# Optimization experiments

Measured on AMD Instinct MI355X. Metric: run time of the kernel, lower is better.

## Reference

```python
import jax, jax.numpy as jnp
import numpy as np
import math

D_MODEL = 1024
FEAT = 16            # feature_dim
HEADS = 16
HEAD_DIM = D_MODEL // HEADS          # 64
EXP = 1 + FEAT + FEAT * FEAT         # 273, expanded (Taylor) feature dim
BATCH = 4
SEQ = 2048


def taylor_exp(x):
    """2nd-order Taylor feature map: [1, x/d^{1/4}, (x ox x)/(sqrt(2)*sqrt(d))]."""
    d = x.shape[-1]
    r2 = math.sqrt(2.0)
    rd = math.sqrt(d)
    rrd = math.sqrt(rd)
    x2 = (x[..., :, None] * x[..., None, :]).reshape(*x.shape[:-1], d * d) / r2
    return jnp.concatenate([jnp.ones_like(x[..., :1]), x / rrd, x2 / rd], axis=-1)


def setup_inputs() -> dict:
    key = jax.random.key(0)
    ks = jax.random.split(key, 9)
    s_in = 1.0 / math.sqrt(D_MODEL)
    inp = {
        "x": jax.random.normal(ks[0], (BATCH, SEQ, D_MODEL), dtype=jnp.float32),
        "kv_state": jnp.zeros((BATCH, HEADS, EXP, HEAD_DIM), dtype=jnp.float32),
        "k_state": jnp.zeros((BATCH, HEADS, EXP), dtype=jnp.float32),
        # Linear params stored as [in, out] (y = x @ W + b)
        "Wq": jax.random.normal(ks[1], (D_MODEL, FEAT * HEADS), dtype=jnp.float32) * s_in,
        "bq": jnp.zeros((FEAT * HEADS,), dtype=jnp.float32),
        "Wk": jax.random.normal(ks[2], (D_MODEL, FEAT * HEADS), dtype=jnp.float32) * s_in,
        "bk": jnp.zeros((FEAT * HEADS,), dtype=jnp.float32),
        "Wv": jax.random.normal(ks[3], (D_MODEL, HEAD_DIM * HEADS), dtype=jnp.float32) * s_in,
        "bv": jnp.zeros((HEAD_DIM * HEADS,), dtype=jnp.float32),
        "Wo": jax.random.normal(ks[4], (HEADS * HEAD_DIM, D_MODEL), dtype=jnp.float32) * s_in,
        "bo": jnp.zeros((D_MODEL,), dtype=jnp.float32),
    }
    return inp


def _forward(x, kv_state, k_state, Wq, bq, Wk, bk, Wv, bv, Wo, bo):
    b, l, _ = x.shape
    # projections -> b h l d
    q = (x @ Wq + bq).reshape(b, l, HEADS, FEAT).transpose(0, 2, 1, 3)
    k = (x @ Wk + bk).reshape(b, l, HEADS, FEAT).transpose(0, 2, 1, 3)
    v = (x @ Wv + bv).reshape(b, l, HEADS, HEAD_DIM).transpose(0, 2, 1, 3)
    q = taylor_exp(q)  # b h l EXP
    k = taylor_exp(k)  # b h l EXP

    # scan over time: carry (kv_state [b,h,EXP,hd], k_state [b,h,EXP])
    qs = jnp.moveaxis(q, 2, 0)  # l b h EXP
    ks = jnp.moveaxis(k, 2, 0)  # l b h EXP
    vs = jnp.moveaxis(v, 2, 0)  # l b h hd

    def step(carry, qkv_t):
        kv, kst = carry
        q_t, k_t, v_t = qkv_t
        kv = kv + k_t[..., :, None] * v_t[..., None, :]   # b h EXP hd
        kst = kst + k_t                                    # b h EXP
        num = jnp.einsum('bhd,bhdc->bhc', q_t, kv)
        den = jnp.einsum('bhd,bhd->bh', q_t, kst) + 1e-6
        return (kv, kst), num / den[..., None]

    (kv_f, kst_f), outs = jax.lax.scan(step, (kv_state, k_state), (qs, ks, vs))
    # outs: l b h hd -> b l (h hd)
    y = jnp.moveaxis(outs, 0, 1).reshape(b, l, HEADS * HEAD_DIM)
    y = y @ Wo + bo  # dropout is identity in eval mode
    return y, kv_f, kst_f


def reference(x, kv_state, k_state, Wq, bq, Wk, bk, Wv, bv, Wo, bo):
    return _forward(x, kv_state, k_state, Wq, bq, Wk, bk, Wv, bv, Wo, bo)
```

## Files before the change

### kernel.cpp

```cpp
#include <hip/hip_runtime.h>

typedef unsigned short u16;
typedef __attribute__((ext_vector_type(8))) short bf16x8;
typedef __attribute__((ext_vector_type(4))) float f32x4;

#define BATCH 4
#define SEQ   2048
#define DM    1024
#define HEADS 16
#define FEAT  16
#define HD    64
#define EXPD  273
#define EXPP  288
#define CHK   128
#define NC    16
#define BH    64
#define QKS   512
#define MROWS 8192
#define C2    0.17677669529663687f

__device__ __forceinline__ u16 f2b(float f) {
  union { float f; unsigned u; } v; v.f = f;
  unsigned u = v.u;
  return (u16)((u + 0x7fffu + ((u >> 16) & 1u)) >> 16);
}
__device__ __forceinline__ float b2f(u16 s) {
  union { unsigned u; float f; } v; v.u = ((unsigned)s) << 16; return v.f;
}
__device__ __forceinline__ unsigned pk2b(float a, float b) {
  unsigned r;
  asm("v_cvt_pk_bf16_f32 %0, %1, %2" : "=v"(r) : "v"(a), "v"(b));
  return r;
}

typedef const unsigned int __attribute__((address_space(1)))* gas1;
typedef unsigned int __attribute__((address_space(3)))* las3;
__device__ __forceinline__ void gl_lds16(const u16* g, u16* l) {
  __builtin_amdgcn_global_load_lds((gas1)(const void*)g, (las3)(void*)l, 16, 0, 0);
}

__global__ __launch_bounds__(256) void prep(const float* __restrict__ x, u16* __restrict__ xb,
                                            const float* __restrict__ Wq, const float* __restrict__ Wk,
                                            const float* __restrict__ Wv, const float* __restrict__ Wo,
                                            u16* __restrict__ wqkvT, u16* __restrict__ woT,
                                            const float* __restrict__ bq, const float* __restrict__ bk,
                                            const float* __restrict__ bv, float* __restrict__ bias_all) {
  __shared__ float tile[32][33];
  int id = blockIdx.x;
  if (id < 8192) {
    int i = id * 256 + threadIdx.x;
    float4 v = ((const float4*)x)[i];
    uint2 r; r.x = pk2b(v.x, v.y); r.y = pk2b(v.z, v.w);
    ((uint2*)xb)[i] = r;
    return;
  }
  id -= 8192;
  if (id < 2560) {
    const float* src; u16* dst; int N, t;
    if (id < 256)       { src = Wq; dst = wqkvT;            N = 256;  t = id; }
    else if (id < 512)  { src = Wk; dst = wqkvT + 256 * DM; N = 256;  t = id - 256; }
    else if (id < 1536) { src = Wv; dst = wqkvT + 512 * DM; N = 1024; t = id - 512; }
    else                { src = Wo; dst = woT;              N = 1024; t = id - 1536; }
    int nt = N / 32;
    int n0 = (t % nt) * 32, k0 = (t / nt) * 32;
    int tx = threadIdx.x & 31, ty = threadIdx.x >> 5;
    for (int i = ty; i < 32; i += 8)
      tile[i][tx] = src[(size_t)(k0 + i) * N + n0 + tx];
    __syncthreads();
    for (int i = ty; i < 32; i += 8)
      dst[(size_t)(n0 + i) * DM + k0 + tx] = f2b(tile[tx][i]);
    return;
  }
  id -= 2560;
  int i = id * 256 + threadIdx.x;
  float v;
  if (i < 256) v = bq[i];
  else if (i < 512) v = bk[i - 256];
  else v = bv[i - 512];
  bias_all[i] = v;
}

__global__ __launch_bounds__(256, 2) void gemmQKV(const u16* __restrict__ A, const u16* __restrict__ BT,
                                                  const float* __restrict__ bias,
                                                  float* __restrict__ qkw, u16* __restrict__ vbT) {
  __shared__ __align__(16) u16 As[2][128 * 32];
  __shared__ __align__(16) u16 Bs[2][192 * 32];
  const int tid = threadIdx.x;
  const int wave = tid >> 6, lane = tid & 63, qd = lane >> 4, ln = lane & 15;
  const int wr = (wave >> 1) * 64, wc = (wave & 1) * 96;
  const int m0 = blockIdx.y * 128, n0 = blockIdx.x * 192;
  const int K = DM;
  f32x4 acc[4][6];
#pragma unroll
  for (int i = 0; i < 4; i++)
#pragma unroll
    for (int j = 0; j < 6; j++) acc[i][j] = (f32x4){0.f, 0.f, 0.f, 0.f};
  const int sr = tid >> 2;
  const int scs = (((tid & 3) ^ ((sr >> 1) & 3))) * 8;
  const u16* gA0 = A + (size_t)(m0 + sr) * K + scs;
  const u16* gA1 = gA0 + (size_t)64 * K;
  const u16* gB0 = BT + (size_t)(n0 + sr) * K + scs;
  auto stage = [&](int buf, int kk) {
    gl_lds16(gA0 + kk, &As[buf][wave * 512]);
    gl_lds16(gA1 + kk, &As[buf][2048 + wave * 512]);
    gl_lds16(gB0 + kk,                   &Bs[buf][wave * 512]);
    gl_lds16(gB0 + (size_t)64 * K + kk,  &Bs[buf][2048 + wave * 512]);
    gl_lds16(gB0 + (size_t)128 * K + kk, &Bs[buf][4096 + wave * 512]);
  };
  const int swz = ((ln >> 1) & 3) << 3;
  auto compute = [&](int buf) {
    bf16x8 af[4], bf[6];
#pragma unroll
    for (int t = 0; t < 4; t++)
      af[t] = *(const bf16x8*)&As[buf][(wr + t * 16 + ln) * 32 + ((qd * 8) ^ swz)];
#pragma unroll
    for (int u = 0; u < 6; u++)
      bf[u] = *(const bf16x8*)&Bs[buf][(wc + u * 16 + ln) * 32 + ((qd * 8) ^ swz)];
#pragma unroll
    for (int mt = 0; mt < 4; mt++)
#pragma unroll
      for (int nt = 0; nt < 6; nt++)
        acc[mt][nt] = __builtin_amdgcn_mfma_f32_16x16x32_bf16(af[mt], bf[nt], acc[mt][nt], 0, 0, 0);
  };
  stage(0, 0);
  int buf = 0;
  for (int kk = 32; kk < K; kk += 32) {
    stage(buf ^ 1, kk);
    asm volatile("s_waitcnt vmcnt(5)" ::: "memory");
    __builtin_amdgcn_s_barrier();
    asm volatile("" ::: "memory");
    compute(buf);
    asm volatile("" ::: "memory");
    __builtin_amdgcn_s_barrier();
    buf ^= 1;
  }
  asm volatile("s_waitcnt vmcnt(0)" ::: "memory");
  __builtin_amdgcn_s_barrier();
  asm volatile("" ::: "memory");
  compute(buf);
#pragma unroll
  for (int nt = 0; nt < 6; nt++) {
    int col = n0 + wc + nt * 16 + ln;
    float bv = bias[col];
    if (col < 512) {
#pragma unroll
      for (int mt = 0; mt < 4; mt++)
#pragma unroll
        for (int r = 0; r < 4; r++) {
          int row = m0 + wr + mt * 16 + qd * 4 + r;
          qkw[(size_t)row * QKS + col] = acc[mt][nt][r] + bv;
        }
    } else {
      int vcol = col - 512;
#pragma unroll
      for (int mt = 0; mt < 4; mt++) {
        uint2 pp;
        pp.x = pk2b(acc[mt][nt][0] + bv, acc[mt][nt][1] + bv);
        pp.y = pk2b(acc[mt][nt][2] + bv, acc[mt][nt][3] + bv);
        int row0 = m0 + wr + mt * 16 + qd * 4;
        *(uint2*)&vbT[(size_t)vcol * MROWS + row0] = pp;
      }
    }
  }
}

__global__ __launch_bounds__(256, 3) void gemm128(const u16* __restrict__ A, const u16* __restrict__ BT,
                                                  const float* __restrict__ bias, int M, int N, int K,
                                                  float* __restrict__ outF) {
  __shared__ __align__(16) u16 As[2][128 * 32];
  __shared__ __align__(16) u16 Bs[2][128 * 32];
  const int tid = threadIdx.x;
  const int wave = tid >> 6, lane = tid & 63, qd = lane >> 4, ln = lane & 15;
  const int wr = (wave >> 1) * 64, wc = (wave & 1) * 64;
  const int m0 = blockIdx.y * 128, n0 = blockIdx.x * 128;
  f32x4 acc[4][4];
#pragma unroll
  for (int i = 0; i < 4; i++)
#pragma unroll
    for (int j = 0; j < 4; j++) acc[i][j] = (f32x4){0.f, 0.f, 0.f, 0.f};
  const int sr = tid >> 2;
  const int scs = (((tid & 3) ^ ((sr >> 1) & 3))) * 8;
  const u16* gA0 = A + (size_t)(m0 + sr) * K + scs;
  const u16* gA1 = gA0 + (size_t)64 * K;
  const u16* gB0 = BT + (size_t)(n0 + sr) * K + scs;
  const u16* gB1 = gB0 + (size_t)64 * K;
  auto stage = [&](int buf, int kk) {
    gl_lds16(gA0 + kk, &As[buf][wave * 512]);
    gl_lds16(gA1 + kk, &As[buf][2048 + wave * 512]);
    gl_lds16(gB0 + kk, &Bs[buf][wave * 512]);
    gl_lds16(gB1 + kk, &Bs[buf][2048 + wave * 512]);
  };
  const int swz = ((ln >> 1) & 3) << 3;
  auto compute = [&](int buf) {
    bf16x8 af[4], bf[4];
#pragma unroll
    for (int t = 0; t < 4; t++)
      af[t] = *(const bf16x8*)&As[buf][(wr + t * 16 + ln) * 32 + ((qd * 8) ^ swz)];
#pragma unroll
    for (int u = 0; u < 4; u++)
      bf[u] = *(const bf16x8*)&Bs[buf][(wc + u * 16 + ln) * 32 + ((qd * 8) ^ swz)];
#pragma unroll
    for (int mt = 0; mt < 4; mt++)
#pragma unroll
      for (int nt = 0; nt < 4; nt++)
        acc[mt][nt] = __builtin_amdgcn_mfma_f32_16x16x32_bf16(af[mt], bf[nt], acc[mt][nt], 0, 0, 0);
  };
  stage(0, 0);
  int buf = 0;
  for (int kk = 32; kk < K; kk += 32) {
    stage(buf ^ 1, kk);
    asm volatile("s_waitcnt vmcnt(4)" ::: "memory");
    __builtin_amdgcn_s_barrier();
    asm volatile("" ::: "memory");
    compute(buf);
    asm volatile("" ::: "memory");
    __builtin_amdgcn_s_barrier();
    buf ^= 1;
  }
  asm volatile("s_waitcnt vmcnt(0)" ::: "memory");
  __builtin_amdgcn_s_barrier();
  asm volatile("" ::: "memory");
  compute(buf);
#pragma unroll
  for (int nt = 0; nt < 4; nt++) {
    int col = n0 + wc + nt * 16 + ln;
    float bv = bias[col];
#pragma unroll
    for (int mt = 0; mt < 4; mt++)
#pragma unroll
      for (int r = 0; r < 4; r++) {
        int row = m0 + wr + mt * 16 + qd * 4 + r;
        outF[(size_t)row * N + col] = acc[mt][nt][r] + bv;
      }
  }
}

template<int KT>
__device__ __forceinline__ void feat_row(const float* q16, int p, u16* dst) {
  float v[16];
  if (KT == 0 && p == 0) {
    v[0] = 1.0f;
#pragma unroll
    for (int j = 1; j < 16; j++) v[j] = 0.5f * q16[j - 1];
  } else if (KT == 0) {
    v[0] = 0.5f * q16[15];
    float wm = C2 * q16[0];
#pragma unroll
    for (int j = 1; j < 16; j++) v[j] = wm * q16[j - 1];
  } else {
    constexpr int c = 2 * KT;
    float wm = C2 * (p ? q16[c]     : q16[c - 1]);
    float w0 = C2 * (p ? q16[c - 1] : q16[c - 2]);
    v[0] = w0 * q16[15];
#pragma unroll
    for (int j = 1; j < 16; j++) v[j] = wm * q16[j - 1];
    if (KT == 8 && p) {
#pragma unroll
      for (int j = 1; j < 16; j++) v[j] = 0.f;
    }
  }
  unsigned w[8];
#pragma unroll
  for (int j = 0; j < 8; j++) w[j] = pk2b(v[2 * j], v[2 * j + 1]);
  *(uint4*)dst = *(uint4*)w;
  *(uint4*)(dst + 8) = *(uint4*)(w + 4);
}

template<int MTB>
__device__ __forceinline__ void kfeat(const float* k16, int p, int t2, u16 (*kfT)[16][136]) {
  float v[16];
  if (MTB == 0) {
    if (p == 0) {
      v[0] = 1.0f;
#pragma unroll
      for (int j = 1; j < 16; j++) v[j] = 0.5f * k16[j - 1];
    } else {
      float w0 = C2 * k16[0], wm = C2 * k16[1];
      v[0] = w0 * k16[15];
#pragma unroll
      for (int j = 1; j < 16; j++) v[j] = wm * k16[j - 1];
    }
  } else if (MTB == 1) {
    if (p == 0) {
      v[0] = 0.5f * k16[15];
      float wm = C2 * k16[0];
#pragma unroll
      for (int j = 1; j < 16; j++) v[j] = wm * k16[j - 1];
    } else {
      float w0 = C2 * k16[1], wm = C2 * k16[2];
      v[0] = w0 * k16[15];
#pragma unroll
      for (int j = 1; j < 16; j++) v[j] = wm * k16[j - 1];
    }
  } else {
    float wm = C2 * (p ? k16[MTB + 1] : k16[MTB - 1]);
    float w0 = C2 * (p ? k16[MTB]     : k16[MTB - 2]);
    v[0] = w0 * k16[15];
#pragma unroll
    for (int j = 1; j < 16; j++) v[j] = wm * k16[j - 1];
  }
  union { unsigned w[8]; u16 s[16]; } u;
#pragma unroll
  for (int j = 0; j < 8; j++) u.w[j] = pk2b(v[2 * j], v[2 * j + 1]);
  int b = 2 * p + (MTB & 1);
#pragma unroll
  for (int el = 0; el < 16; el++) kfT[b][el][t2] = u.s[el];
}

__global__ __launch_bounds__(256) void chunk_sums(const float* __restrict__ qkw, const u16* __restrict__ vbT,
                                                  u16* __restrict__ ckvT, float* __restrict__ ck) {
  __shared__ float kl[CHK][20];
  __shared__ __align__(16) u16 kfT[4][16][136];
  const int tid = threadIdx.x;
  const int bh = blockIdx.x / NC, c = blockIdx.x % NC;
  const int b = bh >> 4, h = bh & 15;
  const int wave = tid >> 6, lane = tid & 63, qd = lane >> 4, ln = lane & 15;
  const int t2 = tid >> 1, p = tid & 1;
  const size_t rowbase = (size_t)(b * SEQ + c * CHK);
  float k16[16];
  {
    const float* kp = &qkw[(rowbase + t2) * QKS + 256 + h * FEAT];
    float4 v0 = *(const float4*)kp, v1 = *(const float4*)(kp + 4);
    float4 v2 = *(const float4*)(kp + 8), v3 = *(const float4*)(kp + 12);
    k16[0] = v0.x; k16[1] = v0.y; k16[2] = v0.z; k16[3] = v0.w;
    k16[4] = v1.x; k16[5] = v1.y; k16[6] = v1.z; k16[7] = v1.w;
    k16[8] = v2.x; k16[9] = v2.y; k16[10] = v2.z; k16[11] = v2.w;
    k16[12] = v3.x; k16[13] = v3.y; k16[14] = v3.z; k16[15] = v3.w;
    float4 h0, h1;
    if (p == 0) { h0 = v0; h1 = v1; } else { h0 = v2; h1 = v3; }
    *(float4*)&kl[t2][p * 8] = h0;
    *(float4*)&kl[t2][p * 8 + 4] = h1;
  }
  uint4 bVv[4][4];
#pragma unroll
  for (int kk2 = 0; kk2 < 4; kk2++)
#pragma unroll
    for (int nt = 0; nt < 4; nt++)
      bVv[kk2][nt] = *(const uint4*)&vbT[(size_t)(h * HD + nt * 16 + ln) * MROWS +
                                         rowbase + kk2 * 32 + qd * 8];
  const size_t obase = (size_t)(bh * NC + c) * HD;
  auto mstore = [&](int mt, int bufw) {
    f32x4 acc[4];
#pragma unroll
    for (int nt = 0; nt < 4; nt++) acc[nt] = (f32x4){0.f, 0.f, 0.f, 0.f};
#pragma unroll
    for (int kk2 = 0; kk2 < 4; kk2++) {
      bf16x8 a = *(const bf16x8*)&kfT[bufw][ln][kk2 * 32 + qd * 8];
#pragma unroll
      for (int nt = 0; nt < 4; nt++) {
        bf16x8 bb = *(const bf16x8*)&bVv[kk2][nt];
        acc[nt] = __builtin_amdgcn_mfma_f32_16x16x32_bf16(a, bb, acc[nt], 0, 0, 0);
      }
    }
#pragma unroll
    for (int nt = 0; nt < 4; nt++) {
      uint2 pp;
      pp.x = pk2b(acc[nt][0], acc[nt][1]);
      pp.y = pk2b(acc[nt][2], acc[nt][3]);
      *(uint2*)&ckvT[(obase + nt * 16 + ln) * EXPP + mt * 16 + qd * 4] = pp;
    }
  };
  __syncthreads();
  kfeat<0>(k16, p, t2, kfT); kfeat<1>(k16, p, t2, kfT);
  __syncthreads();
  mstore(wave, wave);
  __syncthreads();
  kfeat<4>(k16, p, t2, kfT); kfeat<5>(k16, p, t2, kfT);
  __syncthreads();
  mstore(4 + wave, wave);
  __syncthreads();
  kfeat<8>(k16, p, t2, kfT); kfeat<9>(k16, p, t2, kfT);
  __syncthreads();
  mstore(8 + wave, wave);
  __syncthreads();
  kfeat<12>(k16, p, t2, kfT); kfeat<13>(k16, p, t2, kfT);
  __syncthreads();
  mstore(12 + wave, wave);
  __syncthreads();
  {
    float v[16];
    if (p == 0) {
      float w0 = C2 * k16[14], wm = C2 * k16[15];
      v[0] = w0 * k16[15];
#pragma unroll
      for (int j = 1; j < 16; j++) v[j] = wm * k16[j - 1];
    } else {
      v[0] = C2 * k16[15] * k16[15];
#pragma unroll
      for (int j = 1; j < 16; j++) v[j] = 0.f;
    }
    union { unsigned w[8]; u16 s[16]; } u;
#pragma unroll
    for (int j = 0; j < 8; j++) u.w[j] = pk2b(v[2 * j], v[2 * j + 1]);
#pragma unroll
    for (int el = 0; el < 16; el++) kfT[p][el][t2] = u.s[el];
  }
  __syncthreads();
  if (wave < 2) mstore(16 + wave, wave);
  for (int e = tid; e < EXPP; e += 256) {
    float s = 0.f;
    if (e == 0) s = (float)CHK;
    else if (e < 17) { float t = 0.f; for (int tt = 0; tt < CHK; tt++) t += kl[tt][e - 1]; s = 0.5f * t; }
    else if (e < EXPD) {
      int u = e - 17, i0 = u >> 4, j0 = u & 15; float t = 0.f;
      for (int tt = 0; tt < CHK; tt++) t += kl[tt][i0] * kl[tt][j0];
      s = C2 * t;
    }
    ck[(size_t)(bh * NC + c) * EXPP + e] = s;
  }
}

__global__ __launch_bounds__(256) void kv_prefix(u16* __restrict__ ckvT, const float* __restrict__ kv0,
                                                 float* __restrict__ out_kv,
                                                 float* __restrict__ ck, const float* __restrict__ k0,
                                                 float* __restrict__ out_k) {
  const int tid = threadIdx.x;
  const int bh = blockIdx.x / 10, eg = blockIdx.x % 10;
  if (eg == 9) {
    for (int e = tid; e < EXPP; e += 256) {
      float S = (e < EXPD) ? k0[(size_t)bh * EXPD + e] : 0.f;
      for (int c = 0; c < NC; c++) {
        size_t idx = ((size_t)bh * NC + c) * EXPP + e;
        float v = ck[idx];
        ck[idx] = S;
        S += v;
      }
      if (e < EXPD) out_k[(size_t)bh * EXPD + e] = S;
    }
    return;
  }
  const int hd = tid >> 2;
  const int e0 = eg * 32 + (tid & 3) * 8;
  float S[8];
#pragma unroll
  for (int j = 0; j < 8; j++) {
    int e = e0 + j;
    S[j] = (e < EXPD) ? kv0[((size_t)bh * EXPD + e) * HD + hd] : 0.f;
  }
  u16* base = ckvT + ((size_t)bh * NC * HD + hd) * EXPP + e0;
  const size_t cstride = (size_t)HD * EXPP;
  uint4 v0 = *(const uint4*)base;
  uint4 v1 = *(const uint4*)(base + cstride);
  for (int c = 0; c < NC; c++) {
    uint4 vn = v1;
    if (c + 2 < NC) vn = *(const uint4*)(base + (size_t)(c + 2) * cstride);
    union { uint4 q; unsigned w[4]; } pk;
#pragma unroll
    for (int j = 0; j < 4; j++) pk.w[j] = pk2b(S[2 * j], S[2 * j + 1]);
    *(uint4*)(base + (size_t)c * cstride) = pk.q;
    union { uint4 q; u16 s[8]; } vv; vv.q = v0;
#pragma unroll
    for (int j = 0; j < 8; j++) S[j] += b2f(vv.s[j]);
    v0 = v1; v1 = vn;
  }
#pragma unroll
  for (int j = 0; j < 8; j++) {
    int e = e0 + j;
    if (e < EXPD) out_kv[((size_t)bh * EXPD + e) * HD + hd] = S[j];
  }
}

__global__ __launch_bounds__(256) void out_chunk(const float* __restrict__ qkw, const u16* __restrict__ vbT,
                                                 const u16* __restrict__ ckvT, const float* __restrict__ ck,
                                                 u16* __restrict__ ob) {
  __shared__ __align__(16) u16 pool[19456];
  __shared__ float kstl[EXPP];
  __shared__ float denl[CHK];
  u16 (*qlb)[40]  = (u16(*)[40])pool;
  u16 (*klb)[32]  = (u16(*)[32])(pool + 5120);
  u16 (*qfs0)[40] = (u16(*)[40])(pool + 9216);
  u16 (*qfs1)[40] = (u16(*)[40])(pool + 14336);
  u16 (*alB)[72]  = (u16(*)[72])pool;
  u16 (*alA)[72]  = (u16(*)[72])(pool + 9216);
  const int tid = threadIdx.x;
  const int bh = blockIdx.x / NC, c = blockIdx.x % NC;
  const int b = bh >> 4, h = bh & 15;
  const int wave = tid >> 6, lane = tid & 63, qd = lane >> 4, ln = lane & 15;
  const int t2 = tid >> 1, p = tid & 1;
  const size_t rowbase = (size_t)(b * SEQ + c * CHK);
  float q16[16];
  {
    const float* qp = &qkw[(rowbase + t2) * QKS + h * FEAT];
    float4 v0 = *(const float4*)qp, v1 = *(const float4*)(qp + 4);
    float4 v2 = *(const float4*)(qp + 8), v3 = *(const float4*)(qp + 12);
    q16[0] = v0.x; q16[1] = v0.y; q16[2] = v0.z; q16[3] = v0.w;
    q16[4] = v1.x; q16[5] = v1.y; q16[6] = v1.z; q16[7] = v1.w;
    q16[8] = v2.x; q16[9] = v2.y; q16[10] = v2.z; q16[11] = v2.w;
    q16[12] = v3.x; q16[13] = v3.y; q16[14] = v3.z; q16[15] = v3.w;
    unsigned qw[4];
#pragma unroll
    for (int j = 0; j < 4; j++) qw[j] = pk2b(q16[p * 8 + 2 * j], q16[p * 8 + 2 * j + 1]);
    *(uint4*)&qlb[t2][p * 8] = *(uint4*)qw;
    *(uint4*)&qlb[t2][16 + p * 8] = (uint4){0u, 0u, 0u, 0u};
    const float* kp = &qkw[(rowbase + t2) * QKS + 256 + h * FEAT + p * 8];
    float4 k0v = *(const float4*)kp, k1v = *(const float4*)(kp + 4);
    unsigned kw[4] = {pk2b(k0v.x, k0v.y), pk2b(k0v.z, k0v.w),
                      pk2b(k1v.x, k1v.y), pk2b(k1v.z, k1v.w)};
    *(uint4*)&klb[t2][p * 8] = *(uint4*)kw;
    *(uint4*)&klb[t2][16 + p * 8] = (uint4){0u, 0u, 0u, 0u};
  }
  const size_t cbase = (size_t)(bh * NC + c);
  for (int e = tid; e < EXPP; e += 256) kstl[e] = ck[cbase * EXPP + e];
  const u16* sptr = ckvT + (cbase * HD + wave * 16 + ln) * EXPP + qd * 8;
  uint4 bSv[2];
  bSv[0] = *(const uint4*)(sptr + 0 * 32);
  feat_row<0>(q16, p, &qfs0[t2][p * 16]);
  f32x4 accO[8];
#pragma unroll
  for (int nt = 0; nt < 8; nt++) accO[nt] = (f32x4){0.f, 0.f, 0.f, 0.f};
#define KSTEP(KT, CUR, NXT)                                                                \
  {                                                                                        \
    __syncthreads();                                                                       \
    if ((KT) + 1 <= 8) bSv[((KT) + 1) & 1] = *(const uint4*)(sptr + ((KT) + 1) * 32);      \
    bf16x8 bQ0[4];                                                                         \
    _Pragma("unroll")                                                                      \
    for (int nt = 0; nt < 4; nt++) bQ0[nt] = *(const bf16x8*)&CUR[nt * 16 + ln][qd * 8];   \
    feat_row<(KT) + 1>(q16, p, &NXT[t2][p * 16]);                                          \
    bf16x8 aS = *(const bf16x8*)&bSv[(KT) & 1];                                            \
    _Pragma("unroll")                                                                      \
    for (int nt = 0; nt < 4; nt++)                                                         \
      accO[nt] = __builtin_amdgcn_mfma_f32_16x16x32_bf16(aS, bQ0[nt], accO[nt], 0, 0, 0);  \
    _Pragma("unroll")                                                                      \
    for (int nt = 4; nt < 8; nt++) {                                                       \
      bf16x8 bQ1 = *(const bf16x8*)&CUR[nt * 16 + ln][qd * 8];                             \
      accO[nt] = __builtin_amdgcn_mfma_f32_16x16x32_bf16(aS, bQ1, accO[nt], 0, 0, 0);      \
    }                                                                                      \
  }
  KSTEP(0, qfs0, qfs1) KSTEP(1, qfs1, qfs0) KSTEP(2, qfs0, qfs1) KSTEP(3, qfs1, qfs0)
  KSTEP(4, qfs0, qfs1) KSTEP(5, qfs1, qfs0) KSTEP(6, qfs0, qfs1) KSTEP(7, qfs1, qfs0)
#undef KSTEP
  {
    __syncthreads();
    bf16x8 aS = *(const bf16x8*)&bSv[0];
#pragma unroll
    for (int nt = 0; nt < 8; nt++) {
      bf16x8 bQ = *(const bf16x8*)&qfs0[nt * 16 + ln][qd * 8];
      accO[nt] = __builtin_amdgcn_mfma_f32_16x16x32_bf16(aS, bQ, accO[nt], 0, 0, 0);
    }
  }
  __syncthreads();
  float s_poly;
  {
    float s = 0.f;
#pragma unroll
    for (int i2 = 0; i2 < 8; i2++) {
      int i = p * 8 + i2;
      float inner = 0.f;
#pragma unroll
      for (int j = 0; j < 16; j++) inner += q16[j] * kstl[17 + i * 16 + j];
      s += q16[i] * inner;
    }
    s *= C2;
    float s1 = 0.f;
#pragma unroll
    for (int j2 = 0; j2 < 8; j2++) s1 += q16[p * 8 + j2] * kstl[1 + p * 8 + j2];
    s += 0.5f * s1;
    if (p == 0) s += kstl[0] + 1e-6f;
    s_poly = s;
  }
  {
    bf16x8 aK = *(const bf16x8*)&klb[wave * 16 + ln][qd * 8];
#pragma unroll
    for (int nn = 0; nn < 2; nn++) {
      f32x4 accU[4];
#pragma unroll
      for (int j = 0; j < 4; j++) {
        bf16x8 bQ = *(const bf16x8*)&qlb[(nn * 4 + j) * 16 + ln][qd * 8];
        accU[j] = __builtin_amdgcn_mfma_f32_16x16x32_bf16(aK, bQ, (f32x4){0.f, 0.f, 0.f, 0.f}, 0, 0, 0);
      }
#pragma unroll
      for (int j = 0; j < 4; j++) {
        int t = (nn * 4 + j) * 16 + ln, sb = wave * 16 + qd * 4;
        float scm[4];
#pragma unroll
        for (int r = 0; r < 4; r++) {
          float u = accU[j][r];
          float sc = 1.f + 0.25f * u + 0.03125f * u * u;
          scm[r] = (sb + r <= t) ? sc : 0.f;
        }
        uint2 pp; pp.x = pk2b(scm[0], scm[1]); pp.y = pk2b(scm[2], scm[3]);
        *(uint2*)&alA[t][sb] = pp;
      }
    }
  }
  {
    f32x4 accU[8];
    bf16x8 aK = *(const bf16x8*)&klb[(wave + 4) * 16 + ln][qd * 8];
#pragma unroll
    for (int nt = 0; nt < 8; nt++) {
      bf16x8 bQ = *(const bf16x8*)&qlb[nt * 16 + ln][qd * 8];
      accU[nt] = __builtin_amdgcn_mfma_f32_16x16x32_bf16(aK, bQ, (f32x4){0.f, 0.f, 0.f, 0.f}, 0, 0, 0);
    }
    uint4 bVv[4];
#pragma unroll
    for (int kk2 = 0; kk2 < 4; kk2++)
      bVv[kk2] = *(const uint4*)&vbT[(size_t)(h * HD + wave * 16 + ln) * MROWS +
                                     rowbase + kk2 * 32 + qd * 8];
    __syncthreads();
#pragma unroll
    for (int nt = 0; nt < 8; nt++) {
      int t = nt * 16 + ln, sbl = wave * 16 + qd * 4;
      float scm[4];
#pragma unroll
      for (int r = 0; r < 4; r++) {
        float u = accU[nt][r];
        float sc = 1.f + 0.25f * u + 0.03125f * u * u;
        scm[r] = (64 + sbl + r <= t) ? sc : 0.f;
      }
      uint2 pp; pp.x = pk2b(scm[0], scm[1]); pp.y = pk2b(scm[2], scm[3]);
      *(uint2*)&alB[t][sbl] = pp;
    }
    __syncthreads();
#pragma unroll
    for (int kk2 = 0; kk2 < 4; kk2++) {
      bf16x8 aV = *(const bf16x8*)&bVv[kk2];
#pragma unroll
      for (int nt = 0; nt < 8; nt++) {
        bf16x8 bA = (kk2 < 2) ? *(const bf16x8*)&alA[nt * 16 + ln][kk2 * 32 + qd * 8]
                              : *(const bf16x8*)&alB[nt * 16 + ln][(kk2 - 2) * 32 + qd * 8];
        accO[nt] = __builtin_amdgcn_mfma_f32_16x16x32_bf16(aV, bA, accO[nt], 0, 0, 0);
      }
    }
  }
  {
    const u16* arow = p ? &alB[t2][0] : &alA[t2][0];
    float da = 0.f;
#pragma unroll
    for (int sb = 0; sb < 8; sb++) {
      union { uint4 q; u16 hh[8]; } uu;
      uu.q = *(const uint4*)(arow + sb * 8);
#pragma unroll
      for (int j = 0; j < 8; j++) da += b2f(uu.hh[j]);
    }
    float s = s_poly + da;
    s += __shfl_xor(s, 1);
    if (p == 0) denl[t2] = s;
  }
  __syncthreads();
#pragma unroll
  for (int nt = 0; nt < 8; nt++) {
    int t = nt * 16 + ln;
    float rd = 1.0f / denl[t];
    uint2 pp;
    pp.x = pk2b(accO[nt][0] * rd, accO[nt][1] * rd);
    pp.y = pk2b(accO[nt][2] * rd, accO[nt][3] * rd);
    *(uint2*)&ob[(rowbase + t) * DM + h * HD + wave * 16 + qd * 4] = pp;
  }
}

extern "C" void kernel_launch(void* const* d_in, const int* in_sizes, int n_in,
                              void* d_out, int out_size, void* d_ws, size_t ws_size,
                              hipStream_t stream) {
  (void)in_sizes; (void)n_in; (void)out_size;
  const float* x   = (const float*)d_in[0];
  const float* kv0 = (const float*)d_in[1];
  const float* k0  = (const float*)d_in[2];
  const float* bq  = (const float*)d_in[4];
  const float* bk  = (const float*)d_in[6];
  const float* bv  = (const float*)d_in[8];
  const float* bo  = (const float*)d_in[10];
  float* out = (float*)d_out;
  char* ws = (char*)d_ws;
  size_t off = 0;
  auto take = [&](size_t bytes) { char* p = ws + off; off += (bytes + 255) & ~(size_t)255; return p; };
  u16*   xb     = (u16*)  take((size_t)BATCH * SEQ * DM * 2);
  u16*   wqkvT  = (u16*)  take((size_t)1536 * DM * 2);
  u16*   woT    = (u16*)  take((size_t)DM * DM * 2);
  float* bias_a = (float*)take((size_t)1536 * 4);
  float* qkw    = (float*)take((size_t)BATCH * SEQ * QKS * 4);
  u16*   vbT    = (u16*)  take((size_t)BATCH * SEQ * DM * 2);
  u16*   ckvT   = (u16*)  take((size_t)BH * NC * EXPP * HD * 2);
  float* ck     = (float*)take((size_t)BH * NC * EXPP * 4);
  u16*   ob     = (u16*)  take((size_t)BATCH * SEQ * DM * 2);
  if (off > ws_size) return;

  float* out_kv = out + (size_t)BATCH * SEQ * DM;
  float* out_k  = out_kv + (size_t)BH * EXPD * HD;

  prep<<<8192 + 2560 + 6, 256, 0, stream>>>(x, xb,
      (const float*)d_in[3], (const float*)d_in[5], (const float*)d_in[7], (const float*)d_in[9],
      wqkvT, woT, bq, bk, bv, bias_a);

  gemmQKV<<<dim3(8, 64), 256, 0, stream>>>(xb, wqkvT, bias_a, qkw, vbT);

  chunk_sums<<<BH * NC, 256, 0, stream>>>(qkw, vbT, ckvT, ck);
  kv_prefix<<<BH * 10, 256, 0, stream>>>(ckvT, kv0, out_kv, ck, k0, out_k);
  out_chunk<<<BH * NC, 256, 0, stream>>>(qkw, vbT, ckvT, ck, ob);

  gemm128<<<dim3(8, 64), 256, 0, stream>>>(ob, woT, bo, MROWS, DM, DM, out);
}
```

Measured before the change: 274.6 us.

## Quad-buffer Taylor feature tiles in out_chunk and add MFMA priority hints

```diff
diff --git a/kernel.cpp b/kernel.cpp
--- a/kernel.cpp
+++ b/kernel.cpp
@@ -463,15 +463,18 @@
 __global__ __launch_bounds__(256) void out_chunk(const float* __restrict__ qkw, const u16* __restrict__ vbT,
                                                  const u16* __restrict__ ckvT, const float* __restrict__ ck,
                                                  u16* __restrict__ ob) {
-  __shared__ __align__(16) u16 pool[19456];
+  __shared__ __align__(16) u16 pool[25600];
   __shared__ float kstl[EXPP];
   __shared__ float denl[CHK];
-  u16 (*qlb)[40]  = (u16(*)[40])pool;
-  u16 (*klb)[32]  = (u16(*)[32])(pool + 5120);
-  u16 (*qfs0)[40] = (u16(*)[40])(pool + 9216);
-  u16 (*qfs1)[40] = (u16(*)[40])(pool + 14336);
-  u16 (*alB)[72]  = (u16(*)[72])pool;
-  u16 (*alA)[72]  = (u16(*)[72])(pool + 9216);
+  u16 (*qlb)[16] = (u16(*)[16])pool;
+  u16 (*klb)[16] = (u16(*)[16])(pool + 2048);
+  u16* zslab     = pool + 4096;
+  u16 (*qf0)[40] = (u16(*)[40])(pool + 4104);
+  u16 (*qf1)[40] = (u16(*)[40])(pool + 9224);
+  u16 (*qf2)[40] = (u16(*)[40])(pool + 14344);
+  u16 (*qf3)[40] = (u16(*)[40])(pool + 19464);
+  u16 (*alB)[72] = (u16(*)[72])pool;
+  u16 (*alA)[72] = (u16(*)[72])(pool + 9216);
   const int tid = threadIdx.x;
   const int bh = blockIdx.x / NC, c = blockIdx.x % NC;
   const int b = bh >> 4, h = bh & 15;
@@ -491,53 +494,70 @@
 #pragma unroll
     for (int j = 0; j < 4; j++) qw[j] = pk2b(q16[p * 8 + 2 * j], q16[p * 8 + 2 * j + 1]);
     *(uint4*)&qlb[t2][p * 8] = *(uint4*)qw;
-    *(uint4*)&qlb[t2][16 + p * 8] = (uint4){0u, 0u, 0u, 0u};
     const float* kp = &qkw[(rowbase + t2) * QKS + 256 + h * FEAT + p * 8];
     float4 k0v = *(const float4*)kp, k1v = *(const float4*)(kp + 4);
     unsigned kw[4] = {pk2b(k0v.x, k0v.y), pk2b(k0v.z, k0v.w),
                       pk2b(k1v.x, k1v.y), pk2b(k1v.z, k1v.w)};
     *(uint4*)&klb[t2][p * 8] = *(uint4*)kw;
-    *(uint4*)&klb[t2][16 + p * 8] = (uint4){0u, 0u, 0u, 0u};
+    if (tid == 0) *(uint4*)zslab = (uint4){0u, 0u, 0u, 0u};
   }
   const size_t cbase = (size_t)(bh * NC + c);
   for (int e = tid; e < EXPP; e += 256) kstl[e] = ck[cbase * EXPP + e];
   const u16* sptr = ckvT + (cbase * HD + wave * 16 + ln) * EXPP + qd * 8;
-  uint4 bSv[2];
+  uint4 bSv[4];
   bSv[0] = *(const uint4*)(sptr + 0 * 32);
-  feat_row<0>(q16, p, &qfs0[t2][p * 16]);
+  bSv[1] = *(const uint4*)(sptr + 1 * 32);
+  feat_row<0>(q16, p, &qf0[t2][p * 16]);
+  feat_row<1>(q16, p, &qf1[t2][p * 16]);
   f32x4 accO[8];
 #pragma unroll
   for (int nt = 0; nt < 8; nt++) accO[nt] = (f32x4){0.f, 0.f, 0.f, 0.f};
-#define KSTEP(KT, CUR, NXT)                                                                \
+#define CHUNK(KT, QF)                                                                      \
   {                                                                                        \
-    __syncthreads();                                                                       \
-    if ((KT) + 1 <= 8) bSv[((KT) + 1) & 1] = *(const uint4*)(sptr + ((KT) + 1) * 32);      \
-    bf16x8 bQ0[4];                                                                         \
+    bf16x8 aS = *(const bf16x8*)&bSv[(KT) & 3];                                            \
+    bf16x8 bq0[4];                                                                         \
     _Pragma("unroll")                                                                      \
-    for (int nt = 0; nt < 4; nt++) bQ0[nt] = *(const bf16x8*)&CUR[nt * 16 + ln][qd * 8];   \
-    feat_row<(KT) + 1>(q16, p, &NXT[t2][p * 16]);                                          \
-    bf16x8 aS = *(const bf16x8*)&bSv[(KT) & 1];                                            \
+    for (int nt = 0; nt < 4; nt++) bq0[nt] = *(const bf16x8*)&QF[nt * 16 + ln][qd * 8];    \
+    __builtin_amdgcn_s_setprio(1);                                                         \
     _Pragma("unroll")                                                                      \
     for (int nt = 0; nt < 4; nt++)                                                         \
-      accO[nt] = __builtin_amdgcn_mfma_f32_16x16x32_bf16(aS, bQ0[nt], accO[nt], 0, 0, 0);  \
+      accO[nt] = __builtin_amdgcn_mfma_f32_16x16x32_bf16(aS, bq0[nt], accO[nt], 0, 0, 0);  \
     _Pragma("unroll")                                                                      \
     for (int nt = 4; nt < 8; nt++) {                                                       \
-      bf16x8 bQ1 = *(const bf16x8*)&CUR[nt * 16 + ln][qd * 8];                             \
-      accO[nt] = __builtin_amdgcn_mfma_f32_16x16x32_bf16(aS, bQ1, accO[nt], 0, 0, 0);      \
+      bf16x8 bq1 = *(const bf16x8*)&QF[nt * 16 + ln][qd * 8];                              \
+      accO[nt] = __builtin_amdgcn_mfma_f32_16x16x32_bf16(aS, bq1, accO[nt], 0, 0, 0);      \
     }                                                                                      \
-  }
-  KSTEP(0, qfs0, qfs1) KSTEP(1, qfs1, qfs0) KSTEP(2, qfs0, qfs1) KSTEP(3, qfs1, qfs0)
-  KSTEP(4, qfs0, qfs1) KSTEP(5, qfs1, qfs0) KSTEP(6, qfs0, qfs1) KSTEP(7, qfs1, qfs0)
-#undef KSTEP
-  {
-    __syncthreads();
-    bf16x8 aS = *(const bf16x8*)&bSv[0];
-#pragma unroll
-    for (int nt = 0; nt < 8; nt++) {
-      bf16x8 bQ = *(const bf16x8*)&qfs0[nt * 16 + ln][qd * 8];
-      accO[nt] = __builtin_amdgcn_mfma_f32_16x16x32_bf16(aS, bQ, accO[nt], 0, 0, 0);
-    }
-  }
+    __builtin_amdgcn_s_setprio(0);                                                         \
+  }
+  __syncthreads();
+  bSv[2] = *(const uint4*)(sptr + 2 * 32);
+  bSv[3] = *(const uint4*)(sptr + 3 * 32);
+  CHUNK(0, qf0)
+  feat_row<2>(q16, p, &qf2[t2][p * 16]);
+  CHUNK(1, qf1)
+  feat_row<3>(q16, p, &qf3[t2][p * 16]);
+  __syncthreads();
+  bSv[0] = *(const uint4*)(sptr + 4 * 32);
+  bSv[1] = *(const uint4*)(sptr + 5 * 32);
+  CHUNK(2, qf2)
+  feat_row<4>(q16, p, &qf0[t2][p * 16]);
+  CHUNK(3, qf3)
+  feat_row<5>(q16, p, &qf1[t2][p * 16]);
+  __syncthreads();
+  bSv[2] = *(const uint4*)(sptr + 6 * 32);
+  bSv[3] = *(const uint4*)(sptr + 7 * 32);
+  CHUNK(4, qf0)
+  feat_row<6>(q16, p, &qf2[t2][p * 16]);
+  CHUNK(5, qf1)
+  feat_row<7>(q16, p, &qf3[t2][p * 16]);
+  __syncthreads();
+  bSv[0] = *(const uint4*)(sptr + 8 * 32);
+  CHUNK(6, qf2)
+  feat_row<8>(q16, p, &qf0[t2][p * 16]);
+  CHUNK(7, qf3)
+  __syncthreads();
+  CHUNK(8, qf0)
+#undef CHUNK
   __syncthreads();
   float s_poly;
   {
@@ -559,15 +579,19 @@
     s_poly = s;
   }
   {
-    bf16x8 aK = *(const bf16x8*)&klb[wave * 16 + ln][qd * 8];
+    const u16* kap = (qd < 2) ? &klb[wave * 16 + ln][qd * 8] : zslab;
+    bf16x8 aK = *(const bf16x8*)kap;
 #pragma unroll
     for (int nn = 0; nn < 2; nn++) {
       f32x4 accU[4];
+      __builtin_amdgcn_s_setprio(1);
 #pragma unroll
       for (int j = 0; j < 4; j++) {
-        bf16x8 bQ = *(const bf16x8*)&qlb[(nn * 4 + j) * 16 + ln][qd * 8];
+        const u16* qap = (qd < 2) ? &qlb[(nn * 4 + j) * 16 + ln][qd * 8] : zslab;
+        bf16x8 bQ = *(const bf16x8*)qap;
         accU[j] = __builtin_amdgcn_mfma_f32_16x16x32_bf16(aK, bQ, (f32x4){0.f, 0.f, 0.f, 0.f}, 0, 0, 0);
       }
+      __builtin_amdgcn_s_setprio(0);
 #pragma unroll
       for (int j = 0; j < 4; j++) {
         int t = (nn * 4 + j) * 16 + ln, sb = wave * 16 + qd * 4;
@@ -585,12 +609,16 @@
   }
   {
     f32x4 accU[8];
-    bf16x8 aK = *(const bf16x8*)&klb[(wave + 4) * 16 + ln][qd * 8];
+    const u16* kap = (qd < 2) ? &klb[(wave + 4) * 16 + ln][qd * 8] : zslab;
+    bf16x8 aK = *(const bf16x8*)kap;
+    __builtin_amdgcn_s_setprio(1);
 #pragma unroll
     for (int nt = 0; nt < 8; nt++) {
-      bf16x8 bQ = *(const bf16x8*)&qlb[nt * 16 + ln][qd * 8];
+      const u16* qap = (qd < 2) ? &qlb[nt * 16 + ln][qd * 8] : zslab;
+      bf16x8 bQ = *(const bf16x8*)qap;
       accU[nt] = __builtin_amdgcn_mfma_f32_16x16x32_bf16(aK, bQ, (f32x4){0.f, 0.f, 0.f, 0.f}, 0, 0, 0);
     }
+    __builtin_amdgcn_s_setprio(0);
     uint4 bVv[4];
 #pragma unroll
     for (int kk2 = 0; kk2 < 4; kk2++)
@@ -611,6 +639,7 @@
       *(uint2*)&alB[t][sbl] = pp;
     }
     __syncthreads();
+    __builtin_amdgcn_s_setprio(1);
 #pragma unroll
     for (int kk2 = 0; kk2 < 4; kk2++) {
       bf16x8 aV = *(const bf16x8*)&bVv[kk2];
@@ -621,6 +650,7 @@
         accO[nt] = __builtin_amdgcn_mfma_f32_16x16x32_bf16(aV, bA, accO[nt], 0, 0, 0);
       }
     }
+    __builtin_amdgcn_s_setprio(0);
   }
   {
     const u16* arow = p ? &alB[t2][0] : &alA[t2][0];
```

Measured after the change: 269.0 us. 1.02x faster.
